# Kernel optimization log

Measured on AMD Instinct MI355X. Metric: run time of the kernel, lower is better.

The kernel has to match this reference:

```python
import jax, jax.numpy as jnp
import numpy as np

EMBED_DIM = 1024
NUM_HEADS = 16
HEAD_DIM = EMBED_DIM // NUM_HEADS


def setup_inputs() -> dict:
    key = jax.random.key(0)
    kx, kq, kk, kv = jax.random.split(key, 4)
    x = jax.random.normal(kx, (4, 2048, EMBED_DIM), dtype=jnp.float32)
    s = 1.0 / np.sqrt(EMBED_DIM)
    # nn.Linear weight layout: [out, in]; y = x @ W.T
    w_q = jax.random.uniform(kq, (EMBED_DIM, EMBED_DIM), jnp.float32, -s, s)
    w_k = jax.random.uniform(kk, (EMBED_DIM, EMBED_DIM), jnp.float32, -s, s)
    w_v = jax.random.uniform(kv, (EMBED_DIM, EMBED_DIM), jnp.float32, -s, s)
    return {"x": x, "w_q": w_q, "w_k": w_k, "w_v": w_v}


def reference(x, w_q, w_k, w_v):
    B, S, E = x.shape
    H, D = NUM_HEADS, HEAD_DIM
    # projections (Linear without bias): x @ W.T, split into heads
    q = (x @ w_q.T).reshape(B, S, H, D).transpose(0, 2, 1, 3)  # [B,H,S,D]
    k = (x @ w_k.T).reshape(B, S, H, D).transpose(0, 2, 1, 3)  # [B,H,S,D]
    v = (x @ w_v.T).reshape(B, S, H, D).transpose(0, 2, 1, 3)  # [B,H,S,D]
    # NOTE: original scales by sqrt(embed_dim), not sqrt(head_dim)
    scores = jnp.einsum('bhqd,bhkd->bhqk', q, k) / jnp.sqrt(jnp.float32(E))
    attn = jax.nn.softmax(scores, axis=-1)
    out = jnp.einsum('bhqk,bhkd->bhqd', attn, v)
    # concat heads; original forward never applies fc_out
    return out.transpose(0, 2, 1, 3).reshape(B, S, E)
```

## Files before the change

kernel.cpp:

```cpp
#include <hip/hip_runtime.h>
#include <hip/hip_bf16.h>

typedef __hip_bfloat16 bf16;
typedef float f32x4 __attribute__((ext_vector_type(4)));
typedef short bf16x8 __attribute__((ext_vector_type(8)));

#define DI __device__ __forceinline__

constexpr int B_ = 4, S_ = 2048, E_ = 1024, H_ = 16, D_ = 64;
constexpr int M_ = B_ * S_;
constexpr float QSCALE = 0.03125f * 1.4426950408889634f;

DI unsigned short bfbits(float f) {
  __hip_bfloat16 h = __float2bfloat16(f);
  return *reinterpret_cast<unsigned short*>(&h);
}

DI void gload_lds16(const bf16* g, bf16* l) {
  __builtin_amdgcn_global_load_lds((const __attribute__((address_space(1))) void*)g,
                                   (__attribute__((address_space(3))) void*)l, 16, 0, 0);
}

__global__ __launch_bounds__(256) void cast_all(const float* __restrict__ x,
                                                const float* __restrict__ wq,
                                                const float* __restrict__ wk,
                                                const float* __restrict__ wv,
                                                ushort* __restrict__ xb,
                                                ushort* __restrict__ wqb,
                                                ushort* __restrict__ wkb,
                                                ushort* __restrict__ wvb) {
  int id = blockIdx.x * 256 + threadIdx.x;
  const float* src; ushort* dst; int i;
  if (id < 2097152)      { src = x;  dst = xb;  i = id; }
  else if (id < 2359296) { src = wq; dst = wqb; i = id - 2097152; }
  else if (id < 2621440) { src = wk; dst = wkb; i = id - 2359296; }
  else                   { src = wv; dst = wvb; i = id - 2621440; }
  float4 v = reinterpret_cast<const float4*>(src)[i];
  ushort4 o;
  o.x = bfbits(v.x); o.y = bfbits(v.y); o.z = bfbits(v.z); o.w = bfbits(v.w);
  reinterpret_cast<ushort4*>(dst)[i] = o;
}

template <int MODE>
__global__ __launch_bounds__(256) void gemm_qkv(const bf16* __restrict__ A,
                                                const bf16* __restrict__ W,
                                                bf16* __restrict__ dst) {
  constexpr int BM = 128, BN = 128, BK = 32, NK = E_ / BK;
  __shared__ __align__(16) bf16 As[2][BM * BK];
  __shared__ __align__(16) bf16 Bs[2][BN * BK];
  const int t = threadIdx.x;
  const int l = t & 63;
  const int w = t >> 6;
  const int wm = w >> 1, wn = w & 1;
  const int m0 = blockIdx.y * BM, n0 = blockIdx.x * BN;

  f32x4 acc[4][4] = {};

  auto stage = [&](int buf, int kt) {
#pragma unroll
    for (int i = 0; i < 2; ++i) {
      int t2 = i * 256 + t;
      int r = t2 >> 2, sl = t2 & 3;
      int g = sl ^ ((r >> 1) & 3);
      gload_lds16(A + (size_t)(m0 + r) * E_ + kt * BK + g * 8,
                  &As[buf][(size_t)(i * 256 + w * 64) * 8]);
      gload_lds16(W + (size_t)(n0 + r) * E_ + kt * BK + g * 8,
                  &Bs[buf][(size_t)(i * 256 + w * 64) * 8]);
    }
  };

  stage(0, 0);
  int cur = 0;
  for (int kt = 0; kt < NK; ++kt) {
    __syncthreads();
    if (kt + 1 < NK) stage(cur ^ 1, kt + 1);
    bf16x8 af[4], bfr[4];
#pragma unroll
    for (int i = 0; i < 4; ++i) {
      int ra = wm * 64 + i * 16 + (l & 15);
      int sla = (l >> 4) ^ ((ra >> 1) & 3);
      af[i] = *reinterpret_cast<const bf16x8*>(&As[cur][(ra * 4 + sla) * 8]);
      int rb = wn * 64 + i * 16 + (l & 15);
      int slb = (l >> 4) ^ ((rb >> 1) & 3);
      bfr[i] = *reinterpret_cast<const bf16x8*>(&Bs[cur][(rb * 4 + slb) * 8]);
    }
#pragma unroll
    for (int i = 0; i < 4; ++i)
#pragma unroll
      for (int j = 0; j < 4; ++j)
        acc[i][j] = __builtin_amdgcn_mfma_f32_16x16x32_bf16(af[i], bfr[j], acc[i][j], 0, 0, 0);
    cur ^= 1;
  }

  const float oscale = (MODE == 0) ? QSCALE : 1.0f;
#pragma unroll
  for (int i = 0; i < 4; ++i)
#pragma unroll
    for (int j = 0; j < 4; ++j)
#pragma unroll
      for (int jj = 0; jj < 4; ++jj) {
        int mr = m0 + wm * 64 + i * 16 + (l >> 4) * 4 + jj;
        int nc = n0 + wn * 64 + j * 16 + (l & 15);
        int b = mr >> 11, s = mr & 2047, h = nc >> 6, d = nc & 63;
        size_t idx;
        if (MODE == 2) idx = ((size_t)(b * H_ + h) * D_ + d) * S_ + s;
        else           idx = ((size_t)(b * H_ + h) * S_ + s) * D_ + d;
        dst[idx] = __float2bfloat16(acc[i][j][jj] * oscale);
      }
}

__global__ __launch_bounds__(256) void attn_kernel(const bf16* __restrict__ Q,
                                                   const bf16* __restrict__ K,
                                                   const bf16* __restrict__ Vt,
                                                   float* __restrict__ out) {
  constexpr int KT = 64, NT = S_ / KT;
  __shared__ __align__(16) bf16 Ks[2][KT * D_];
  __shared__ __align__(16) bf16 Vs[2][D_ * KT];
  __shared__ __align__(16) bf16 Ps[4][16 * KT];

  const int t = threadIdx.x, l = t & 63, w = t >> 6;
  const int hi = l >> 4, r15 = l & 15;
  const int p = blockIdx.x;
  const int lg = (p & 7) * 256 + (p >> 3);
  const int qblk = lg & 31, h = (lg >> 5) & 15, b = lg >> 9;
  const int q0 = qblk * 64 + w * 16;
  const size_t bh = (size_t)(b * H_ + h);
  const bf16* Qb = Q + bh * S_ * D_;
  const bf16* Kb = K + bh * S_ * D_;
  const bf16* Vb = Vt + bh * D_ * S_;

  bf16x8 aq[2];
#pragma unroll
  for (int c = 0; c < 2; ++c)
    aq[c] = *reinterpret_cast<const bf16x8*>(Qb + (size_t)(q0 + r15) * D_ + c * 32 + hi * 8);

  f32x4 o_acc[4] = {};
  float lsum[4] = {0.f, 0.f, 0.f, 0.f};

  auto stage = [&](int buf, int kt) {
    const bf16* Kt_ = Kb + (size_t)kt * KT * D_;
    const bf16* Vt_ = Vb + kt * KT;
#pragma unroll
    for (int i = 0; i < 2; ++i) {
      int idx = i * 256 + t;
      int rr = idx >> 3, s = idx & 7;
      int g = s ^ (rr & 7);
      gload_lds16(Kt_ + rr * D_ + g * 8, &Ks[buf][(i * 256 + w * 64) * 8]);
      gload_lds16(Vt_ + (size_t)rr * S_ + g * 8, &Vs[buf][(i * 256 + w * 64) * 8]);
    }
  };

  stage(0, 0);
  int cur = 0;
  for (int kt = 0; kt < NT; ++kt) {
    __syncthreads();
    if (kt + 1 < NT) stage(cur ^ 1, kt + 1);

    f32x4 sc[4] = {};
#pragma unroll
    for (int c = 0; c < 2; ++c)
#pragma unroll
      for (int nt = 0; nt < 4; ++nt) {
        int r = nt * 16 + r15;
        bf16x8 bk = *reinterpret_cast<const bf16x8*>(
            &Ks[cur][r * D_ + (((4 * c + hi) ^ (r & 7)) * 8)]);
        sc[nt] = __builtin_amdgcn_mfma_f32_16x16x32_bf16(aq[c], bk, sc[nt], 0, 0, 0);
      }

    bf16* Pw = Ps[w];
#pragma unroll
    for (int nt = 0; nt < 4; ++nt)
#pragma unroll
      for (int jj = 0; jj < 4; ++jj) {
        float pf = __builtin_amdgcn_exp2f(sc[nt][jj]);
        lsum[jj] += pf;
        int q = hi * 4 + jj;
        int blk = 2 * nt + (r15 >> 3);
        Pw[q * KT + ((blk ^ (q & 7)) * 8) + (r15 & 7)] = __float2bfloat16(pf);
      }
    asm volatile("s_waitcnt lgkmcnt(0)" ::: "memory");

#pragma unroll
    for (int c = 0; c < 2; ++c) {
      bf16x8 ap = *reinterpret_cast<const bf16x8*>(
          &Pw[r15 * KT + (((4 * c + hi) ^ (r15 & 7)) * 8)]);
#pragma unroll
      for (int nt = 0; nt < 4; ++nt) {
        int d = nt * 16 + r15;
        bf16x8 bv = *reinterpret_cast<const bf16x8*>(
            &Vs[cur][d * KT + (((4 * c + hi) ^ (d & 7)) * 8)]);
        o_acc[nt] = __builtin_amdgcn_mfma_f32_16x16x32_bf16(ap, bv, o_acc[nt], 0, 0, 0);
      }
    }
    cur ^= 1;
  }

#pragma unroll
  for (int jj = 0; jj < 4; ++jj) {
    float s = lsum[jj];
    s += __shfl_xor(s, 1);
    s += __shfl_xor(s, 2);
    s += __shfl_xor(s, 4);
    s += __shfl_xor(s, 8);
    lsum[jj] = 1.f / s;
  }
#pragma unroll
  for (int nt = 0; nt < 4; ++nt)
#pragma unroll
    for (int jj = 0; jj < 4; ++jj) {
      int q = q0 + hi * 4 + jj;
      int d = nt * 16 + r15;
      out[((size_t)b * S_ + q) * E_ + h * D_ + d] = o_acc[nt][jj] * lsum[jj];
    }
}

extern "C" void kernel_launch(void* const* d_in, const int* in_sizes, int n_in,
                              void* d_out, int out_size, void* d_ws, size_t ws_size,
                              hipStream_t stream) {
  const float* x = (const float*)d_in[0];
  const float* wq = (const float*)d_in[1];
  const float* wk = (const float*)d_in[2];
  const float* wv = (const float*)d_in[3];
  float* out = (float*)d_out;
  char* ws = (char*)d_ws;

  bf16* xb  = (bf16*)(ws + 0);
  bf16* wqb = (bf16*)(ws + 16777216);
  bf16* wkb = (bf16*)(ws + 18874368);
  bf16* wvb = (bf16*)(ws + 20971520);
  bf16* Qh  = (bf16*)(ws + 23068672);
  bf16* Kh  = (bf16*)(ws + 39845888);
  bf16* Vth = (bf16*)(ws + 56623104);

  cast_all<<<11264, 256, 0, stream>>>(x, wq, wk, wv, (ushort*)xb, (ushort*)wqb,
                                      (ushort*)wkb, (ushort*)wvb);

  dim3 gg(E_ / 128, M_ / 128);
  gemm_qkv<0><<<gg, 256, 0, stream>>>(xb, wqb, Qh);
  gemm_qkv<1><<<gg, 256, 0, stream>>>(xb, wkb, Kh);
  gemm_qkv<2><<<gg, 256, 0, stream>>>(xb, wvb, Vth);

  attn_kernel<<<2048, 256, 0, stream>>>(Qh, Kh, Vth, out);
}
```

Before: 303.6 us.

## Fuse QKV GEMMs into one launch and keep softmax probabilities in registers

Merges the three projection GEMM launches into one 1536-block kernel that picks Q, K or V from the block index, using XCD-aware tile mapping. In attention it computes S transposed (K as the A operand), so each lane's exp'd scores can be packed with v_cvt_pk_bf16 straight into the P operand. This drops the LDS round trip through Ps and its waitcnt. V is read as two 4-element halves so it matches the register-resident P layout. Both loops are unrolled by two with fixed buffers and precomputed LDS offsets. The risks are the extra V LDS reads and a cross-lane shuffle to redistribute the row sums.

```diff
diff --git a/kernel.cpp b/kernel.cpp
--- a/kernel.cpp
+++ b/kernel.cpp
@@ -4,6 +4,8 @@
 typedef __hip_bfloat16 bf16;
 typedef float f32x4 __attribute__((ext_vector_type(4)));
 typedef short bf16x8 __attribute__((ext_vector_type(8)));
+typedef short bf16x4 __attribute__((ext_vector_type(4)));
+typedef unsigned u32x4 __attribute__((ext_vector_type(4)));
 
 #define DI __device__ __forceinline__
 
@@ -14,6 +16,12 @@
 DI unsigned short bfbits(float f) {
   __hip_bfloat16 h = __float2bfloat16(f);
   return *reinterpret_cast<unsigned short*>(&h);
+}
+
+DI unsigned cvt_pk_bf16(float lo, float hi) {
+  unsigned r;
+  asm("v_cvt_pk_bf16_f32 %0, %1, %2" : "=v"(r) : "v"(lo), "v"(hi));
+  return r;
 }
 
 DI void gload_lds16(const bf16* g, bf16* l) {
@@ -41,18 +49,26 @@
   reinterpret_cast<ushort4*>(dst)[i] = o;
 }
 
-template <int MODE>
-__global__ __launch_bounds__(256) void gemm_qkv(const bf16* __restrict__ A,
-                                                const bf16* __restrict__ W,
-                                                bf16* __restrict__ dst) {
+__global__ __launch_bounds__(256) void gemm_qkv_fused(const bf16* __restrict__ A,
+                                                      const bf16* __restrict__ Wq,
+                                                      const bf16* __restrict__ Wk,
+                                                      const bf16* __restrict__ Wv,
+                                                      bf16* __restrict__ Qh,
+                                                      bf16* __restrict__ Kh,
+                                                      bf16* __restrict__ Vth) {
   constexpr int BM = 128, BN = 128, BK = 32, NK = E_ / BK;
   __shared__ __align__(16) bf16 As[2][BM * BK];
   __shared__ __align__(16) bf16 Bs[2][BN * BK];
-  const int t = threadIdx.x;
-  const int l = t & 63;
-  const int w = t >> 6;
+  const int t = threadIdx.x, l = t & 63, w = t >> 6;
   const int wm = w >> 1, wn = w & 1;
-  const int m0 = blockIdx.y * BM, n0 = blockIdx.x * BN;
+
+  const int bid = blockIdx.x;
+  const int xcd = bid & 7, jq = bid >> 3;
+  const int m0 = (xcd * 8 + (jq & 7)) * BM;
+  const int ntile = jq >> 3;
+  const int sec = ntile >> 3;
+  const int n0 = (ntile & 7) * BN;
+  const bf16* W = sec == 0 ? Wq : (sec == 1 ? Wk : Wv);
 
   f32x4 acc[4][4] = {};
 
@@ -69,30 +85,36 @@
     }
   };
 
-  stage(0, 0);
-  int cur = 0;
-  for (int kt = 0; kt < NK; ++kt) {
-    __syncthreads();
-    if (kt + 1 < NK) stage(cur ^ 1, kt + 1);
+  auto tile = [&](int buf) {
     bf16x8 af[4], bfr[4];
 #pragma unroll
     for (int i = 0; i < 4; ++i) {
       int ra = wm * 64 + i * 16 + (l & 15);
       int sla = (l >> 4) ^ ((ra >> 1) & 3);
-      af[i] = *reinterpret_cast<const bf16x8*>(&As[cur][(ra * 4 + sla) * 8]);
+      af[i] = *reinterpret_cast<const bf16x8*>(&As[buf][(ra * 4 + sla) * 8]);
       int rb = wn * 64 + i * 16 + (l & 15);
       int slb = (l >> 4) ^ ((rb >> 1) & 3);
-      bfr[i] = *reinterpret_cast<const bf16x8*>(&Bs[cur][(rb * 4 + slb) * 8]);
+      bfr[i] = *reinterpret_cast<const bf16x8*>(&Bs[buf][(rb * 4 + slb) * 8]);
     }
 #pragma unroll
     for (int i = 0; i < 4; ++i)
 #pragma unroll
       for (int j = 0; j < 4; ++j)
         acc[i][j] = __builtin_amdgcn_mfma_f32_16x16x32_bf16(af[i], bfr[j], acc[i][j], 0, 0, 0);
-    cur ^= 1;
+  };
+
+  stage(0, 0);
+  for (int kt = 0; kt < NK; kt += 2) {
+    __syncthreads();
+    if (kt + 1 < NK) stage(1, kt + 1);
+    tile(0);
+    __syncthreads();
+    if (kt + 2 < NK) stage(0, kt + 2);
+    tile(1);
   }
 
-  const float oscale = (MODE == 0) ? QSCALE : 1.0f;
+  const float oscale = (sec == 0) ? QSCALE : 1.0f;
+  bf16* dst = sec == 0 ? Qh : (sec == 1 ? Kh : Vth);
 #pragma unroll
   for (int i = 0; i < 4; ++i)
 #pragma unroll
@@ -103,8 +125,8 @@
         int nc = n0 + wn * 64 + j * 16 + (l & 15);
         int b = mr >> 11, s = mr & 2047, h = nc >> 6, d = nc & 63;
         size_t idx;
-        if (MODE == 2) idx = ((size_t)(b * H_ + h) * D_ + d) * S_ + s;
-        else           idx = ((size_t)(b * H_ + h) * S_ + s) * D_ + d;
+        if (sec == 2) idx = ((size_t)(b * H_ + h) * D_ + d) * S_ + s;
+        else          idx = ((size_t)(b * H_ + h) * S_ + s) * D_ + d;
         dst[idx] = __float2bfloat16(acc[i][j][jj] * oscale);
       }
 }
@@ -116,7 +138,6 @@
   constexpr int KT = 64, NT = S_ / KT;
   __shared__ __align__(16) bf16 Ks[2][KT * D_];
   __shared__ __align__(16) bf16 Vs[2][D_ * KT];
-  __shared__ __align__(16) bf16 Ps[4][16 * KT];
 
   const int t = threadIdx.x, l = t & 63, w = t >> 6;
   const int hi = l >> 4, r15 = l & 15;
@@ -134,8 +155,23 @@
   for (int c = 0; c < 2; ++c)
     aq[c] = *reinterpret_cast<const bf16x8*>(Qb + (size_t)(q0 + r15) * D_ + c * 32 + hi * 8);
 
+  int koff[2][4], voff[2][4][2];
+#pragma unroll
+  for (int c = 0; c < 2; ++c)
+#pragma unroll
+    for (int nt = 0; nt < 4; ++nt) {
+      int r = nt * 16 + r15;
+      koff[c][nt] = (r * D_ + ((4 * c + hi) ^ (r & 7)) * 8) * 2;
+      int d = nt * 16 + r15;
+#pragma unroll
+      for (int hf = 0; hf < 2; ++hf) {
+        int blk = 4 * c + 2 * hf + (hi >> 1);
+        voff[c][nt][hf] = (d * KT + ((blk ^ (d & 7)) * 8) + 4 * (hi & 1)) * 2;
+      }
+    }
+
   f32x4 o_acc[4] = {};
-  float lsum[4] = {0.f, 0.f, 0.f, 0.f};
+  float lsum = 0.f;
 
   auto stage = [&](int buf, int kt) {
     const bf16* Kt_ = Kb + (size_t)kt * KT * D_;
@@ -150,68 +186,66 @@
     }
   };
 
+  auto tile = [&](int buf) {
+    const char* kbase = (const char*)Ks[buf];
+    const char* vbase = (const char*)Vs[buf];
+    f32x4 sc[4] = {};
+#pragma unroll
+    for (int c = 0; c < 2; ++c)
+#pragma unroll
+      for (int nt = 0; nt < 4; ++nt) {
+        bf16x8 bk = *reinterpret_cast<const bf16x8*>(kbase + koff[c][nt]);
+        sc[nt] = __builtin_amdgcn_mfma_f32_16x16x32_bf16(bk, aq[c], sc[nt], 0, 0, 0);
+      }
+    u32x4 pa[2];
+#pragma unroll
+    for (int nt = 0; nt < 4; ++nt) {
+      float pf0 = __builtin_amdgcn_exp2f(sc[nt][0]);
+      float pf1 = __builtin_amdgcn_exp2f(sc[nt][1]);
+      float pf2 = __builtin_amdgcn_exp2f(sc[nt][2]);
+      float pf3 = __builtin_amdgcn_exp2f(sc[nt][3]);
+      lsum += (pf0 + pf1) + (pf2 + pf3);
+      pa[nt >> 1][(nt & 1) * 2 + 0] = cvt_pk_bf16(pf0, pf1);
+      pa[nt >> 1][(nt & 1) * 2 + 1] = cvt_pk_bf16(pf2, pf3);
+    }
+#pragma unroll
+    for (int c = 0; c < 2; ++c) {
+      bf16x8 ap = __builtin_bit_cast(bf16x8, pa[c]);
+#pragma unroll
+      for (int nt = 0; nt < 4; ++nt) {
+        bf16x4 v0 = *reinterpret_cast<const bf16x4*>(vbase + voff[c][nt][0]);
+        bf16x4 v1 = *reinterpret_cast<const bf16x4*>(vbase + voff[c][nt][1]);
+        bf16x8 bv;
+#pragma unroll
+        for (int e = 0; e < 4; ++e) { bv[e] = v0[e]; bv[e + 4] = v1[e]; }
+        o_acc[nt] = __builtin_amdgcn_mfma_f32_16x16x32_bf16(ap, bv, o_acc[nt], 0, 0, 0);
+      }
+    }
+  };
+
   stage(0, 0);
-  int cur = 0;
-  for (int kt = 0; kt < NT; ++kt) {
-    __syncthreads();
-    if (kt + 1 < NT) stage(cur ^ 1, kt + 1);
-
-    f32x4 sc[4] = {};
-#pragma unroll
-    for (int c = 0; c < 2; ++c)
-#pragma unroll
-      for (int nt = 0; nt < 4; ++nt) {
-        int r = nt * 16 + r15;
-        bf16x8 bk = *reinterpret_cast<const bf16x8*>(
-            &Ks[cur][r * D_ + (((4 * c + hi) ^ (r & 7)) * 8)]);
-        sc[nt] = __builtin_amdgcn_mfma_f32_16x16x32_bf16(aq[c], bk, sc[nt], 0, 0, 0);
-      }
-
-    bf16* Pw = Ps[w];
-#pragma unroll
-    for (int nt = 0; nt < 4; ++nt)
-#pragma unroll
-      for (int jj = 0; jj < 4; ++jj) {
-        float pf = __builtin_amdgcn_exp2f(sc[nt][jj]);
-        lsum[jj] += pf;
-        int q = hi * 4 + jj;
-        int blk = 2 * nt + (r15 >> 3);
-        Pw[q * KT + ((blk ^ (q & 7)) * 8) + (r15 & 7)] = __float2bfloat16(pf);
-      }
-    asm volatile("s_waitcnt lgkmcnt(0)" ::: "memory");
-
-#pragma unroll
-    for (int c = 0; c < 2; ++c) {
-      bf16x8 ap = *reinterpret_cast<const bf16x8*>(
-          &Pw[r15 * KT + (((4 * c + hi) ^ (r15 & 7)) * 8)]);
-#pragma unroll
-      for (int nt = 0; nt < 4; ++nt) {
-        int d = nt * 16 + r15;
-        bf16x8 bv = *reinterpret_cast<const bf16x8*>(
-            &Vs[cur][d * KT + (((4 * c + hi) ^ (d & 7)) * 8)]);
-        o_acc[nt] = __builtin_amdgcn_mfma_f32_16x16x32_bf16(ap, bv, o_acc[nt], 0, 0, 0);
-      }
-    }
-    cur ^= 1;
+  for (int kt = 0; kt < NT; kt += 2) {
+    __syncthreads();
+    if (kt + 1 < NT) stage(1, kt + 1);
+    tile(0);
+    __syncthreads();
+    if (kt + 2 < NT) stage(0, kt + 2);
+    tile(1);
   }
 
+  lsum += __shfl_xor(lsum, 16);
+  lsum += __shfl_xor(lsum, 32);
+  float inv = 1.f / lsum;
 #pragma unroll
   for (int jj = 0; jj < 4; ++jj) {
-    float s = lsum[jj];
-    s += __shfl_xor(s, 1);
-    s += __shfl_xor(s, 2);
-    s += __shfl_xor(s, 4);
-    s += __shfl_xor(s, 8);
-    lsum[jj] = 1.f / s;
+    float invj = __shfl(inv, (l & 48) + hi * 4 + jj);
+    int q = q0 + hi * 4 + jj;
+#pragma unroll
+    for (int nt = 0; nt < 4; ++nt) {
+      int d = nt * 16 + r15;
+      out[((size_t)b * S_ + q) * E_ + h * D_ + d] = o_acc[nt][jj] * invj;
+    }
   }
-#pragma unroll
-  for (int nt = 0; nt < 4; ++nt)
-#pragma unroll
-    for (int jj = 0; jj < 4; ++jj) {
-      int q = q0 + hi * 4 + jj;
-      int d = nt * 16 + r15;
-      out[((size_t)b * S_ + q) * E_ + h * D_ + d] = o_acc[nt][jj] * lsum[jj];
-    }
 }
 
 extern "C" void kernel_launch(void* const* d_in, const int* in_sizes, int n_in,
@@ -235,10 +269,7 @@
   cast_all<<<11264, 256, 0, stream>>>(x, wq, wk, wv, (ushort*)xb, (ushort*)wqb,
                                       (ushort*)wkb, (ushort*)wvb);
 
-  dim3 gg(E_ / 128, M_ / 128);
-  gemm_qkv<0><<<gg, 256, 0, stream>>>(xb, wqb, Qh);
-  gemm_qkv<1><<<gg, 256, 0, stream>>>(xb, wkb, Kh);
-  gemm_qkv<2><<<gg, 256, 0, stream>>>(xb, wvb, Vth);
+  gemm_qkv_fused<<<1536, 256, 0, stream>>>(xb, wqb, wkb, wvb, Qh, Kh, Vth);
 
   attn_kernel<<<2048, 256, 0, stream>>>(Qh, Kh, Vth, out);
 }
```

Result: faster. 278.7 us (-8.2%).
